# Performance work log

Hardware: AMD Instinct MI355X
Metric: run time of the kernel (lower is better)

## Reference

```python
import jax, jax.numpy as jnp
import numpy as np

E = 8        # n_routed_experts
Z = 4        # zero_expert_num (identity experts)
K = 2        # moe_topk
SCALE = 2.5  # routed_scaling_factor
T, H, I = 8192, 1024, 512


def setup_inputs() -> dict:
    key = jax.random.key(0)
    k0, k1, k2, k3, k4 = jax.random.split(key, 5)
    return {
        "hidden_states": jax.random.normal(k0, (T, H), jnp.float32),
        "router_w": jax.random.normal(k1, (E + Z, H), jnp.float32) * 0.02,
        "correction_bias": jax.random.normal(k2, (E + Z,), jnp.float32) * 0.01,
        "w13": jax.random.normal(k3, (E, 2 * I, H), jnp.float32) * 0.02,
        "w2": jax.random.normal(k4, (E, H, I), jnp.float32) * 0.02,
    }


def reference(hidden_states, router_w, correction_bias, w13, w2):
    # ---- router (float32) ----
    logits = hidden_states.astype(jnp.float32) @ router_w.T          # [T, E+Z]
    scores = jax.nn.softmax(logits, axis=-1)
    # correction bias only affects expert *selection*, not the gate weights
    _, topk_idx = jax.lax.top_k(scores + correction_bias, K)          # [T, K]
    topk_w = jnp.take_along_axis(scores, topk_idx, axis=-1)          # renormalize=False

    # ---- zero experts (identity type): idx >= E contributes scale * x ----
    is_zero = topk_idx >= E                                           # [T, K]
    routed_w = jnp.where(is_zero, 0.0, topk_w)
    zero_scale = jnp.where(is_zero, topk_w, 0.0).sum(-1, keepdims=True)
    zero_result = zero_scale * hidden_states                          # [T, H]

    # ---- combine weights per routed expert: [T, E] ----
    tok = jnp.arange(hidden_states.shape[0])[:, None]
    safe_idx = jnp.clip(topk_idx, 0, E - 1)   # zero-expert slots carry weight 0
    combine = jnp.zeros((hidden_states.shape[0], E), scores.dtype)
    combine = combine.at[tok, safe_idx].add(routed_w)

    # ---- grouped expert GEMMs (SiLU gated MLP), combined densely ----
    h = jnp.einsum('th,eih->eti', hidden_states, w13)                 # [E, T, 2I]
    g, u = jnp.split(h, 2, axis=-1)
    act = jax.nn.silu(g) * u                                          # [E, T, I]
    eo = jnp.einsum('eti,ehi->eth', act, w2)                          # [E, T, H]
    routed = jnp.einsum('te,eth->th', combine, eo)                    # [T, H]

    return routed * SCALE + zero_result
```

## Files before the change

### kernel.cpp

```cpp
#include <hip/hip_runtime.h>
#include <hip/hip_bf16.h>
#include <math.h>

typedef __bf16 bf16_t;
typedef bf16_t bf16x8 __attribute__((ext_vector_type(8)));
typedef float f32x4 __attribute__((ext_vector_type(4)));

#define T_TOK 8192
#define HDIM  1024
#define IDIM  512
#define NEXP  8
#define NTOT  12
#define MAXROWS (2 * T_TOK + NEXP * 128)
#define MAX_MTILES (MAXROWS / 128)

__device__ __forceinline__ void gll16(const bf16_t* g, bf16_t* l) {
  __builtin_amdgcn_global_load_lds((__attribute__((address_space(1))) void*)g,
                                   (__attribute__((address_space(3))) void*)l,
                                   16, 0, 0);
}

__global__ void cast_bf16_kernel(const float* __restrict__ in, bf16_t* __restrict__ out,
                                 size_t n8) {
  size_t gid = (size_t)blockIdx.x * blockDim.x + threadIdx.x;
  if (gid >= n8) return;
  size_t i = gid * 8;
  float4 a = *(const float4*)&in[i];
  float4 b = *(const float4*)&in[i + 4];
  bf16x8 o;
  o[0] = (bf16_t)a.x; o[1] = (bf16_t)a.y; o[2] = (bf16_t)a.z; o[3] = (bf16_t)a.w;
  o[4] = (bf16_t)b.x; o[5] = (bf16_t)b.y; o[6] = (bf16_t)b.z; o[7] = (bf16_t)b.w;
  *(bf16x8*)&out[i] = o;
}

__global__ void router_kernel(const float* __restrict__ x, const float* __restrict__ rw,
                              const float* __restrict__ bias,
                              int* __restrict__ tk_e, float* __restrict__ tk_w,
                              float* __restrict__ zscale) {
  int t = blockIdx.x;
  int l = threadIdx.x;
  const float4* xr = (const float4*)(x + (size_t)t * HDIM);
  float4 xv[4];
#pragma unroll
  for (int i = 0; i < 4; i++) xv[i] = xr[l + 64 * i];
  float part[NTOT];
#pragma unroll
  for (int e = 0; e < NTOT; e++) {
    const float4* wr = (const float4*)(rw + (size_t)e * HDIM);
    float s = 0.f;
#pragma unroll
    for (int i = 0; i < 4; i++) {
      float4 w = wr[l + 64 * i];
      s += xv[i].x * w.x + xv[i].y * w.y + xv[i].z * w.z + xv[i].w * w.w;
    }
    part[e] = s;
  }
#pragma unroll
  for (int off = 32; off > 0; off >>= 1)
#pragma unroll
    for (int e = 0; e < NTOT; e++) part[e] += __shfl_down(part[e], off);

  if (l == 0) {
    float mx = part[0];
#pragma unroll
    for (int e = 1; e < NTOT; e++) mx = fmaxf(mx, part[e]);
    float p[NTOT], den = 0.f;
#pragma unroll
    for (int e = 0; e < NTOT; e++) { p[e] = expf(part[e] - mx); den += p[e]; }
    float inv = 1.f / den;
#pragma unroll
    for (int e = 0; e < NTOT; e++) p[e] *= inv;
    float s0 = -1e30f, s1 = -1e30f; int i0 = 0, i1 = 0;
#pragma unroll
    for (int e = 0; e < NTOT; e++) {
      float v = p[e] + bias[e];
      if (v > s0) { s1 = s0; i1 = i0; s0 = v; i0 = e; }
      else if (v > s1) { s1 = v; i1 = e; }
    }
    float zs = 0.f;
    int idx[2] = { i0, i1 };
#pragma unroll
    for (int k = 0; k < 2; k++) {
      int e = idx[k];
      float w = p[e];
      if (e >= NEXP) { zs += w; tk_e[2 * t + k] = -1; tk_w[2 * t + k] = 0.f; }
      else           { tk_e[2 * t + k] = e; tk_w[2 * t + k] = w; }
    }
    zscale[t] = zs;
  }
}

__global__ void zero_init_kernel(int* __restrict__ counts, int* __restrict__ sel_tok,
                                 float* __restrict__ sel_w) {
  int i = blockIdx.x * blockDim.x + threadIdx.x;
  if (i < MAXROWS) { sel_tok[i] = 0; sel_w[i] = 0.f; }
  if (i < NEXP) counts[i] = 0;
}

__global__ void count_kernel(const int* __restrict__ tk_e, int* __restrict__ counts) {
  __shared__ int lc[NEXP];
  int tid = threadIdx.x;
  if (tid < NEXP) lc[tid] = 0;
  __syncthreads();
  int t = blockIdx.x * blockDim.x + tid;
  int e0 = tk_e[2 * t], e1 = tk_e[2 * t + 1];
  if (e0 >= 0) atomicAdd(&lc[e0], 1);
  if (e1 >= 0) atomicAdd(&lc[e1], 1);
  __syncthreads();
  if (tid < NEXP) atomicAdd(&counts[tid], lc[tid]);
}

__global__ void scan_kernel(const int* __restrict__ counts, int* __restrict__ off_pad,
                            int* __restrict__ cursor, int* __restrict__ total_rows,
                            int* __restrict__ tile_e, int* __restrict__ tile_p0,
                            int* __restrict__ n_mtiles) {
  if (threadIdx.x == 0) {
    int run = 0, nt = 0;
    for (int e = 0; e < NEXP; e++) {
      off_pad[e] = run;
      cursor[e] = run;
      int ntile = (counts[e] + 127) / 128;
      for (int i = 0; i < ntile; i++) {
        tile_e[nt] = e;
        tile_p0[nt] = run + i * 128;
        nt++;
      }
      run += ntile * 128;
    }
    *total_rows = run;
    *n_mtiles = nt;
  }
}

__global__ void assign_kernel(const int* __restrict__ tk_e, const float* __restrict__ tk_w,
                              int* __restrict__ cursor, int* __restrict__ sel_tok,
                              float* __restrict__ sel_w, int* __restrict__ pos) {
  __shared__ int lc[NEXP];
  __shared__ int lbase[NEXP];
  int tid = threadIdx.x;
  if (tid < NEXP) lc[tid] = 0;
  __syncthreads();
  int t = blockIdx.x * blockDim.x + tid;
  int e0 = tk_e[2 * t], e1 = tk_e[2 * t + 1];
  int r0 = (e0 >= 0) ? atomicAdd(&lc[e0], 1) : -1;
  int r1 = (e1 >= 0) ? atomicAdd(&lc[e1], 1) : -1;
  __syncthreads();
  if (tid < NEXP) lbase[tid] = atomicAdd(&cursor[tid], lc[tid]);
  __syncthreads();
  int p0 = -1, p1 = -1;
  if (e0 >= 0) { p0 = lbase[e0] + r0; sel_tok[p0] = t; sel_w[p0] = 2.5f * tk_w[2 * t]; }
  if (e1 >= 0) { p1 = lbase[e1] + r1; sel_tok[p1] = t; sel_w[p1] = 2.5f * tk_w[2 * t + 1]; }
  pos[2 * t] = p0;
  pos[2 * t + 1] = p1;
}

__global__ void gather_cast_kernel(const float* __restrict__ x, const int* __restrict__ sel_tok,
                                   const int* __restrict__ total_rows, bf16_t* __restrict__ xg) {
  size_t gid = (size_t)blockIdx.x * blockDim.x + threadIdx.x;
  size_t p = gid >> 7;
  if (p >= (size_t)*total_rows) return;
  size_t j = (gid & 127) << 3;
  int t = sel_tok[p];
  float4 a = *(const float4*)&x[(size_t)t * HDIM + j];
  float4 b = *(const float4*)&x[(size_t)t * HDIM + j + 4];
  bf16x8 o;
  o[0] = (bf16_t)a.x; o[1] = (bf16_t)a.y; o[2] = (bf16_t)a.z; o[3] = (bf16_t)a.w;
  o[4] = (bf16_t)b.x; o[5] = (bf16_t)b.y; o[6] = (bf16_t)b.z; o[7] = (bf16_t)b.w;
  *(bf16x8*)&xg[p * HDIM + j] = o;
}

__global__ __launch_bounds__(256) void gemm1_kernel(
    const bf16_t* __restrict__ xg, const bf16_t* __restrict__ w13b,
    const int* __restrict__ tile_e, const int* __restrict__ tile_p0,
    const int* __restrict__ n_mtiles, bf16_t* __restrict__ actb) {
  const int ti = blockIdx.x;
  if (ti >= *n_mtiles) return;
  const int e = tile_e[ti];
  const int p0 = tile_p0[ti];
  const int g0 = blockIdx.y * 64;

  __shared__ alignas(16) bf16_t As[128 * 32];
  __shared__ alignas(16) bf16_t Bs[128 * 32];
  const int tid = threadIdx.x;
  const int w = tid >> 6, l = tid & 63;
  const int wr = w >> 1, wc = w & 1;
  const int quad = l >> 4, c16 = l & 15;

  const int sr = w * 32 + (l >> 2);
  const int sc = (l & 3) * 8;
  const bf16_t* Ag0 = xg + (size_t)(p0 + sr) * HDIM + sc;
  const bf16_t* w13e = w13b + (size_t)e * (2 * IDIM) * HDIM;
  int r0 = sr, r1 = sr + 16;
  int col0 = g0 + (r0 >> 6) * 32 + (((r0 >> 4) & 1) * 16) + (r0 & 15) + (((r0 >> 5) & 1) ? IDIM : 0);
  int col1 = g0 + (r1 >> 6) * 32 + (((r1 >> 4) & 1) * 16) + (r1 & 15) + (((r1 >> 5) & 1) ? IDIM : 0);
  const bf16_t* Bg0 = w13e + (size_t)col0 * HDIM + sc;
  const bf16_t* Bg1 = w13e + (size_t)col1 * HDIM + sc;
  bf16_t* Al0 = &As[(w * 32) * 32];
  bf16_t* Bl0 = &Bs[(w * 32) * 32];

  f32x4 acc[4][4];
#pragma unroll
  for (int i = 0; i < 4; i++)
#pragma unroll
    for (int j = 0; j < 4; j++) acc[i][j] = (f32x4){0.f, 0.f, 0.f, 0.f};

  for (int k0 = 0; k0 < HDIM; k0 += 32) {
    gll16(Ag0 + k0, Al0);
    gll16(Ag0 + k0 + (size_t)16 * HDIM, Al0 + 16 * 32);
    gll16(Bg0 + k0, Bl0);
    gll16(Bg1 + k0, Bl0 + 16 * 32);
    __syncthreads();
    bf16x8 af[4], bfv[4];
#pragma unroll
    for (int mt = 0; mt < 4; mt++)
      af[mt] = *(const bf16x8*)&As[(wr * 64 + mt * 16 + c16) * 32 + quad * 8];
#pragma unroll
    for (int nt = 0; nt < 4; nt++)
      bfv[nt] = *(const bf16x8*)&Bs[(wc * 64 + nt * 16 + c16) * 32 + quad * 8];
#pragma unroll
    for (int mt = 0; mt < 4; mt++)
#pragma unroll
      for (int nt = 0; nt < 4; nt++)
        acc[mt][nt] = __builtin_amdgcn_mfma_f32_16x16x32_bf16(af[mt], bfv[nt], acc[mt][nt], 0, 0, 0);
    __syncthreads();
  }

#pragma unroll
  for (int mt = 0; mt < 4; mt++) {
    int rowb = p0 + wr * 64 + mt * 16 + quad * 4;
#pragma unroll
    for (int nt = 0; nt < 2; nt++) {
      int col = g0 + wc * 32 + nt * 16 + c16;
#pragma unroll
      for (int r = 0; r < 4; r++) {
        float g = acc[mt][nt][r];
        float u = acc[mt][nt + 2][r];
        float s = g / (1.f + expf(-g));
        actb[(size_t)(rowb + r) * IDIM + col] = (bf16_t)(s * u);
      }
    }
  }
}

__global__ __launch_bounds__(256) void gemm2_kernel(
    const bf16_t* __restrict__ actb, const bf16_t* __restrict__ w2b,
    const float* __restrict__ sel_w, const int* __restrict__ tile_e,
    const int* __restrict__ tile_p0, const int* __restrict__ n_mtiles,
    bf16_t* __restrict__ eob) {
  const int ti = blockIdx.x;
  if (ti >= *n_mtiles) return;
  const int e = tile_e[ti];
  const int p0 = tile_p0[ti];
  const int n0 = blockIdx.y * 128;

  __shared__ alignas(16) bf16_t As[128 * 32];
  __shared__ alignas(16) bf16_t Bs[128 * 32];
  const int tid = threadIdx.x;
  const int w = tid >> 6, l = tid & 63;
  const int wr = w >> 1, wc = w & 1;
  const int quad = l >> 4, c16 = l & 15;

  const int sr = w * 32 + (l >> 2);
  const int sc = (l & 3) * 8;
  const bf16_t* Ag0 = actb + (size_t)(p0 + sr) * IDIM + sc;
  const bf16_t* Bg0 = w2b + (size_t)e * HDIM * IDIM + (size_t)(n0 + sr) * IDIM + sc;
  bf16_t* Al0 = &As[(w * 32) * 32];
  bf16_t* Bl0 = &Bs[(w * 32) * 32];

  f32x4 acc[4][4];
#pragma unroll
  for (int i = 0; i < 4; i++)
#pragma unroll
    for (int j = 0; j < 4; j++) acc[i][j] = (f32x4){0.f, 0.f, 0.f, 0.f};

  for (int k0 = 0; k0 < IDIM; k0 += 32) {
    gll16(Ag0 + k0, Al0);
    gll16(Ag0 + k0 + (size_t)16 * IDIM, Al0 + 16 * 32);
    gll16(Bg0 + k0, Bl0);
    gll16(Bg0 + k0 + (size_t)16 * IDIM, Bl0 + 16 * 32);
    __syncthreads();
    bf16x8 af[4], bfv[4];
#pragma unroll
    for (int mt = 0; mt < 4; mt++)
      af[mt] = *(const bf16x8*)&As[(wr * 64 + mt * 16 + c16) * 32 + quad * 8];
#pragma unroll
    for (int nt = 0; nt < 4; nt++)
      bfv[nt] = *(const bf16x8*)&Bs[(wc * 64 + nt * 16 + c16) * 32 + quad * 8];
#pragma unroll
    for (int mt = 0; mt < 4; mt++)
#pragma unroll
      for (int nt = 0; nt < 4; nt++)
        acc[mt][nt] = __builtin_amdgcn_mfma_f32_16x16x32_bf16(af[mt], bfv[nt], acc[mt][nt], 0, 0, 0);
    __syncthreads();
  }

#pragma unroll
  for (int mt = 0; mt < 4; mt++) {
    int rowb = wr * 64 + mt * 16 + quad * 4;
    float cw[4];
#pragma unroll
    for (int r = 0; r < 4; r++) cw[r] = sel_w[p0 + rowb + r];
#pragma unroll
    for (int nt = 0; nt < 4; nt++) {
      int col = n0 + wc * 64 + nt * 16 + c16;
#pragma unroll
      for (int r = 0; r < 4; r++)
        eob[(size_t)(p0 + rowb + r) * HDIM + col] = (bf16_t)(cw[r] * acc[mt][nt][r]);
    }
  }
}

__global__ void combine_kernel(const float* __restrict__ x, const float* __restrict__ zscale,
                               const int* __restrict__ pos, const bf16_t* __restrict__ eob,
                               float* __restrict__ out) {
  size_t gid = (size_t)blockIdx.x * blockDim.x + threadIdx.x;
  size_t t = gid >> 7;
  size_t j = (gid & 127) << 3;
  float zs = zscale[t];
  int p0 = pos[2 * t], p1 = pos[2 * t + 1];
  float4 a = *(const float4*)&x[t * HDIM + j];
  float4 b = *(const float4*)&x[t * HDIM + j + 4];
  float o[8] = { zs * a.x, zs * a.y, zs * a.z, zs * a.w,
                 zs * b.x, zs * b.y, zs * b.z, zs * b.w };
  if (p0 >= 0) {
    bf16x8 v = *(const bf16x8*)&eob[(size_t)p0 * HDIM + j];
#pragma unroll
    for (int k = 0; k < 8; k++) o[k] += (float)v[k];
  }
  if (p1 >= 0) {
    bf16x8 v = *(const bf16x8*)&eob[(size_t)p1 * HDIM + j];
#pragma unroll
    for (int k = 0; k < 8; k++) o[k] += (float)v[k];
  }
  *(float4*)&out[t * HDIM + j] = make_float4(o[0], o[1], o[2], o[3]);
  *(float4*)&out[t * HDIM + j + 4] = make_float4(o[4], o[5], o[6], o[7]);
}

extern "C" void kernel_launch(void* const* d_in, const int* in_sizes, int n_in,
                              void* d_out, int out_size, void* d_ws, size_t ws_size,
                              hipStream_t stream) {
  const float* x    = (const float*)d_in[0];
  const float* rw   = (const float*)d_in[1];
  const float* bias = (const float*)d_in[2];
  const float* w13  = (const float*)d_in[3];
  const float* w2   = (const float*)d_in[4];
  float* out = (float*)d_out;

  char* ws = (char*)d_ws;
  bf16_t* w13b = (bf16_t*)ws;  ws += (size_t)NEXP * 2 * IDIM * HDIM * 2;
  bf16_t* w2b  = (bf16_t*)ws;  ws += (size_t)NEXP * HDIM * IDIM * 2;
  bf16_t* xg   = (bf16_t*)ws;  ws += (size_t)MAXROWS * HDIM * 2;
  bf16_t* actb = (bf16_t*)ws;  ws += (size_t)MAXROWS * IDIM * 2;
  bf16_t* eob  = (bf16_t*)ws;  ws += (size_t)MAXROWS * HDIM * 2;
  int*   tk_e    = (int*)ws;   ws += (size_t)T_TOK * 2 * 4;
  float* tk_w    = (float*)ws; ws += (size_t)T_TOK * 2 * 4;
  float* zscale  = (float*)ws; ws += (size_t)T_TOK * 4;
  int*   pos     = (int*)ws;   ws += (size_t)T_TOK * 2 * 4;
  int*   sel_tok = (int*)ws;   ws += (size_t)MAXROWS * 4;
  float* sel_w   = (float*)ws; ws += (size_t)MAXROWS * 4;
  int*   counts  = (int*)ws;   ws += NEXP * 4;
  int*   off_pad = (int*)ws;   ws += NEXP * 4;
  int*   cursor  = (int*)ws;   ws += NEXP * 4;
  int*   total_rows = (int*)ws; ws += 4;
  int*   tile_e  = (int*)ws;   ws += MAX_MTILES * 4;
  int*   tile_p0 = (int*)ws;   ws += MAX_MTILES * 4;
  int*   n_mtiles = (int*)ws;  ws += 4;

  {
    size_t n8 = (size_t)NEXP * 2 * IDIM * HDIM / 8;
    cast_bf16_kernel<<<(n8 + 255) / 256, 256, 0, stream>>>(w13, w13b, n8);
    n8 = (size_t)NEXP * HDIM * IDIM / 8;
    cast_bf16_kernel<<<(n8 + 255) / 256, 256, 0, stream>>>(w2, w2b, n8);
  }
  router_kernel<<<T_TOK, 64, 0, stream>>>(x, rw, bias, tk_e, tk_w, zscale);
  zero_init_kernel<<<(MAXROWS + 255) / 256, 256, 0, stream>>>(counts, sel_tok, sel_w);
  count_kernel<<<T_TOK / 256, 256, 0, stream>>>(tk_e, counts);
  scan_kernel<<<1, 64, 0, stream>>>(counts, off_pad, cursor, total_rows,
                                    tile_e, tile_p0, n_mtiles);
  assign_kernel<<<T_TOK / 256, 256, 0, stream>>>(tk_e, tk_w, cursor, sel_tok, sel_w, pos);
  gather_cast_kernel<<<(size_t)MAXROWS * (HDIM / 8) / 256, 256, 0, stream>>>(
      x, sel_tok, total_rows, xg);

  gemm1_kernel<<<dim3(MAX_MTILES, IDIM / 64), 256, 0, stream>>>(
      xg, w13b, tile_e, tile_p0, n_mtiles, actb);
  gemm2_kernel<<<dim3(MAX_MTILES, HDIM / 128), 256, 0, stream>>>(
      actb, w2b, sel_w, tile_e, tile_p0, n_mtiles, eob);

  combine_kernel<<<(size_t)T_TOK * HDIM / 8 / 256, 256, 0, stream>>>(
      x, zscale, pos, eob, out);
}
```

Measured before the change: 235.6 us.

## Triple-buffer LDS with async prefetch and XOR swizzle in expert GEMMs

```diff
diff --git a/kernel.cpp b/kernel.cpp
--- a/kernel.cpp
+++ b/kernel.cpp
@@ -179,15 +179,16 @@
   const int p0 = tile_p0[ti];
   const int g0 = blockIdx.y * 64;
 
-  __shared__ alignas(16) bf16_t As[128 * 32];
-  __shared__ alignas(16) bf16_t Bs[128 * 32];
+  __shared__ alignas(16) bf16_t As[3 * 128 * 32];
+  __shared__ alignas(16) bf16_t Bs[3 * 128 * 32];
   const int tid = threadIdx.x;
   const int w = tid >> 6, l = tid & 63;
   const int wr = w >> 1, wc = w & 1;
   const int quad = l >> 4, c16 = l & 15;
+  const int qs = quad ^ ((c16 >> 1) & 3);
 
   const int sr = w * 32 + (l >> 2);
-  const int sc = (l & 3) * 8;
+  const int sc = ((l & 3) ^ ((l >> 3) & 3)) * 8;
   const bf16_t* Ag0 = xg + (size_t)(p0 + sr) * HDIM + sc;
   const bf16_t* w13e = w13b + (size_t)e * (2 * IDIM) * HDIM;
   int r0 = sr, r1 = sr + 16;
@@ -195,8 +196,7 @@
   int col1 = g0 + (r1 >> 6) * 32 + (((r1 >> 4) & 1) * 16) + (r1 & 15) + (((r1 >> 5) & 1) ? IDIM : 0);
   const bf16_t* Bg0 = w13e + (size_t)col0 * HDIM + sc;
   const bf16_t* Bg1 = w13e + (size_t)col1 * HDIM + sc;
-  bf16_t* Al0 = &As[(w * 32) * 32];
-  bf16_t* Bl0 = &Bs[(w * 32) * 32];
+  const int stoff = (w * 32) * 32;
 
   f32x4 acc[4][4];
 #pragma unroll
@@ -204,25 +204,40 @@
 #pragma unroll
     for (int j = 0; j < 4; j++) acc[i][j] = (f32x4){0.f, 0.f, 0.f, 0.f};
 
-  for (int k0 = 0; k0 < HDIM; k0 += 32) {
-    gll16(Ag0 + k0, Al0);
-    gll16(Ag0 + k0 + (size_t)16 * HDIM, Al0 + 16 * 32);
-    gll16(Bg0 + k0, Bl0);
-    gll16(Bg1 + k0, Bl0 + 16 * 32);
-    __syncthreads();
+  auto stage = [&](int buf, int kk) {
+    gll16(Ag0 + kk, &As[buf + stoff]);
+    gll16(Ag0 + kk + (size_t)16 * HDIM, &As[buf + stoff + 16 * 32]);
+    gll16(Bg0 + kk, &Bs[buf + stoff]);
+    gll16(Bg1 + kk, &Bs[buf + stoff + 16 * 32]);
+  };
+  auto compute = [&](int buf) {
     bf16x8 af[4], bfv[4];
 #pragma unroll
     for (int mt = 0; mt < 4; mt++)
-      af[mt] = *(const bf16x8*)&As[(wr * 64 + mt * 16 + c16) * 32 + quad * 8];
+      af[mt] = *(const bf16x8*)&As[buf + (wr * 64 + mt * 16 + c16) * 32 + qs * 8];
 #pragma unroll
     for (int nt = 0; nt < 4; nt++)
-      bfv[nt] = *(const bf16x8*)&Bs[(wc * 64 + nt * 16 + c16) * 32 + quad * 8];
+      bfv[nt] = *(const bf16x8*)&Bs[buf + (wc * 64 + nt * 16 + c16) * 32 + qs * 8];
 #pragma unroll
     for (int mt = 0; mt < 4; mt++)
 #pragma unroll
       for (int nt = 0; nt < 4; nt++)
         acc[mt][nt] = __builtin_amdgcn_mfma_f32_16x16x32_bf16(af[mt], bfv[nt], acc[mt][nt], 0, 0, 0);
-    __syncthreads();
+  };
+
+  constexpr int NT = HDIM / 32;
+  int b0 = 0, b1 = 128 * 32, b2 = 2 * 128 * 32;
+  stage(b0, 0);
+  stage(b1, 32);
+  asm volatile("s_waitcnt vmcnt(4)" ::: "memory");
+  __builtin_amdgcn_s_barrier();
+  for (int t = 0; t < NT; ++t) {
+    if (t + 2 < NT) stage(b2, (t + 2) * 32);
+    compute(b0);
+    if (t + 2 < NT) { asm volatile("s_waitcnt vmcnt(4) lgkmcnt(0)" ::: "memory"); }
+    else            { asm volatile("s_waitcnt vmcnt(0) lgkmcnt(0)" ::: "memory"); }
+    if (t + 1 < NT) __builtin_amdgcn_s_barrier();
+    int tb = b0; b0 = b1; b1 = b2; b2 = tb;
   }
 
 #pragma unroll
@@ -253,19 +268,19 @@
   const int p0 = tile_p0[ti];
   const int n0 = blockIdx.y * 128;
 
-  __shared__ alignas(16) bf16_t As[128 * 32];
-  __shared__ alignas(16) bf16_t Bs[128 * 32];
+  __shared__ alignas(16) bf16_t As[3 * 128 * 32];
+  __shared__ alignas(16) bf16_t Bs[3 * 128 * 32];
   const int tid = threadIdx.x;
   const int w = tid >> 6, l = tid & 63;
   const int wr = w >> 1, wc = w & 1;
   const int quad = l >> 4, c16 = l & 15;
+  const int qs = quad ^ ((c16 >> 1) & 3);
 
   const int sr = w * 32 + (l >> 2);
-  const int sc = (l & 3) * 8;
+  const int sc = ((l & 3) ^ ((l >> 3) & 3)) * 8;
   const bf16_t* Ag0 = actb + (size_t)(p0 + sr) * IDIM + sc;
   const bf16_t* Bg0 = w2b + (size_t)e * HDIM * IDIM + (size_t)(n0 + sr) * IDIM + sc;
-  bf16_t* Al0 = &As[(w * 32) * 32];
-  bf16_t* Bl0 = &Bs[(w * 32) * 32];
+  const int stoff = (w * 32) * 32;
 
   f32x4 acc[4][4];
 #pragma unroll
@@ -273,25 +288,40 @@
 #pragma unroll
     for (int j = 0; j < 4; j++) acc[i][j] = (f32x4){0.f, 0.f, 0.f, 0.f};
 
-  for (int k0 = 0; k0 < IDIM; k0 += 32) {
-    gll16(Ag0 + k0, Al0);
-    gll16(Ag0 + k0 + (size_t)16 * IDIM, Al0 + 16 * 32);
-    gll16(Bg0 + k0, Bl0);
-    gll16(Bg0 + k0 + (size_t)16 * IDIM, Bl0 + 16 * 32);
-    __syncthreads();
+  auto stage = [&](int buf, int kk) {
+    gll16(Ag0 + kk, &As[buf + stoff]);
+    gll16(Ag0 + kk + (size_t)16 * IDIM, &As[buf + stoff + 16 * 32]);
+    gll16(Bg0 + kk, &Bs[buf + stoff]);
+    gll16(Bg0 + kk + (size_t)16 * IDIM, &Bs[buf + stoff + 16 * 32]);
+  };
+  auto compute = [&](int buf) {
     bf16x8 af[4], bfv[4];
 #pragma unroll
     for (int mt = 0; mt < 4; mt++)
-      af[mt] = *(const bf16x8*)&As[(wr * 64 + mt * 16 + c16) * 32 + quad * 8];
+      af[mt] = *(const bf16x8*)&As[buf + (wr * 64 + mt * 16 + c16) * 32 + qs * 8];
 #pragma unroll
     for (int nt = 0; nt < 4; nt++)
-      bfv[nt] = *(const bf16x8*)&Bs[(wc * 64 + nt * 16 + c16) * 32 + quad * 8];
+      bfv[nt] = *(const bf16x8*)&Bs[buf + (wc * 64 + nt * 16 + c16) * 32 + qs * 8];
 #pragma unroll
     for (int mt = 0; mt < 4; mt++)
 #pragma unroll
       for (int nt = 0; nt < 4; nt++)
         acc[mt][nt] = __builtin_amdgcn_mfma_f32_16x16x32_bf16(af[mt], bfv[nt], acc[mt][nt], 0, 0, 0);
-    __syncthreads();
+  };
+
+  constexpr int NT = IDIM / 32;
+  int b0 = 0, b1 = 128 * 32, b2 = 2 * 128 * 32;
+  stage(b0, 0);
+  stage(b1, 32);
+  asm volatile("s_waitcnt vmcnt(4)" ::: "memory");
+  __builtin_amdgcn_s_barrier();
+  for (int t = 0; t < NT; ++t) {
+    if (t + 2 < NT) stage(b2, (t + 2) * 32);
+    compute(b0);
+    if (t + 2 < NT) { asm volatile("s_waitcnt vmcnt(4) lgkmcnt(0)" ::: "memory"); }
+    else            { asm volatile("s_waitcnt vmcnt(0) lgkmcnt(0)" ::: "memory"); }
+    if (t + 1 < NT) __builtin_amdgcn_s_barrier();
+    int tb = b0; b0 = b1; b1 = b2; b2 = tb;
   }
 
 #pragma unroll
```

New measurement: 242.9 us. +3.1%, slower.
